# Performance work log

Measured on AMD Instinct MI355X. Metric: run time of the kernel, lower is better.

Reference implementation:

```python
import jax, jax.numpy as jnp
import numpy as np

K = 2          # kernel_size
STRIDE = 1
C_IN = 2       # n_channels (hardcoded in module)
NQ = K * K     # 4 qubits
PI = np.pi


def _apply_1q(state, gate, wire):
    # state: [N, 16] complex64; gate: [N,2,2] (batched) or [2,2] (shared)
    N = state.shape[0]
    s = state.reshape((N,) + (2,) * NQ)
    s = jnp.moveaxis(s, 1 + wire, NQ)          # wire axis -> last
    s = s.reshape(N, -1, 2)
    if gate.ndim == 3:
        s = jnp.einsum('nab,nkb->nka', gate, s)
    else:
        s = jnp.einsum('ab,nkb->nka', gate, s)
    s = s.reshape((N,) + (2,) * NQ)
    s = jnp.moveaxis(s, NQ, 1 + wire)
    return s.reshape(N, -1)


def _apply_cnot(state, ctrl, tgt):
    N = state.shape[0]
    s = state.reshape((N,) + (2,) * NQ)
    s = jnp.moveaxis(s, (1 + ctrl, 1 + tgt), (NQ - 1, NQ))
    shp = s.shape
    s = s.reshape(N, -1, 2, 2)                 # [..., ctrl, tgt]
    s = jnp.concatenate([s[:, :, :1, :], s[:, :, 1:, ::-1]], axis=2)
    s = s.reshape(shp)
    s = jnp.moveaxis(s, (NQ - 1, NQ), (1 + ctrl, 1 + tgt))
    return s.reshape(N, -1)


def _rx(theta):
    # theta: [N] or scalar -> [N,2,2] or [2,2] complex
    c = jnp.cos(theta / 2).astype(jnp.complex64)
    s = (-1j) * jnp.sin(theta / 2).astype(jnp.complex64)
    return jnp.stack([jnp.stack([c, s], -1), jnp.stack([s, c], -1)], -2)


def _ry(theta):
    c = jnp.cos(theta / 2)
    s = jnp.sin(theta / 2)
    return jnp.stack([jnp.stack([c, -s], -1), jnp.stack([s, c], -1)], -2).astype(jnp.complex64)


def _circuit(angles, weights):
    # angles: [N, 8]; weights: [L, 4]. Returns expval(PauliZ) per wire: [N, 4].
    N = angles.shape[0]
    state = jnp.zeros((N, 2 ** NQ), jnp.complex64).at[:, 0].set(1.0)
    for i in range(NQ):
        state = _apply_1q(state, _rx(angles[:, 2 * i]), i)
        state = _apply_1q(state, _ry(angles[:, 2 * i + 1]), i)
    # BasicEntanglerLayers: per layer RX(w[l,i]) on wire i, then CNOT ring
    for l in range(weights.shape[0]):
        for i in range(NQ):
            state = _apply_1q(state, _rx(weights[l, i]), i)
        for i in range(NQ):
            state = _apply_cnot(state, i, (i + 1) % NQ)
    p = state.real ** 2 + state.imag ** 2
    p = p.reshape((N,) + (2,) * NQ)
    ez = [jnp.sum(jnp.take(p, 0, axis=1 + w) - jnp.take(p, 1, axis=1 + w),
                  axis=tuple(range(1, NQ))) for w in range(NQ)]
    return jnp.stack(ez, -1)


def _forward(x, weights):
    B, C, H, W = x.shape
    nh = (H - K) // STRIDE + 1
    nw = (W - K) // STRIDE + 1
    # unfold: [B, C, nh, nw, K*K] with patch-element order (kh, kw)
    subs = [x[:, :, kh:kh + (nh - 1) * STRIDE + 1:STRIDE,
                    kw:kw + (nw - 1) * STRIDE + 1:STRIDE]
            for kh in range(K) for kw in range(K)]
    patches = jnp.stack(subs, axis=-1)                      # [B,C,nh,nw,KK]
    patches = patches.transpose(0, 2, 3, 4, 1)              # [B,nh,nw,KK,C]
    patches = patches.reshape(B, nh * nw, K * K * C)
    # per-sample min-max normalize to [0, pi]
    flat = patches.reshape(B, -1)
    pmin = flat.min(axis=1)[:, None, None]
    pmax = flat.max(axis=1)[:, None, None]
    angles = (patches - pmin) / (pmax - pmin + 1e-8) * PI
    angles = angles.reshape(B * nh * nw, K * K * C)
    out = _circuit(angles, weights)                         # [B*nh*nw, 4]
    return out.reshape(B, nh, nw, NQ).transpose(0, 3, 1, 2)


def setup_inputs() -> dict:
    key = jax.random.key(0)
    k1, k2 = jax.random.split(key)
    x = jax.random.normal(k1, (8, C_IN, 224, 224), dtype=jnp.float32)
    weights = jax.random.uniform(k2, (1, NQ), dtype=jnp.float32) * (2 * PI)
    return {"x": x, "weights": weights}


def reference(x, weights):
    return _forward(x, weights)
```

## Files before the change

### kernel.cpp

```cpp
#include <hip/hip_runtime.h>
#include <math.h>

#define BATCH 8
#define CIN   2
#define H     224
#define W     224
#define NH    223
#define NW    223
#define PIXB  (H * W)
#define NPB   (CIN * H * W)
#define PER_B (NH * NW)
#define NBPB  ((PER_B + 255) / 256)
#define BPB   32
#define PI_F  3.14159265358979323846f

__global__ __launch_bounds__(256) void minmax_kernel(
        const float* __restrict__ x, float* __restrict__ ws) {
    int b  = blockIdx.x / BPB;
    int cb = blockIdx.x % BPB;
    const float4* xb = (const float4*)(x + (size_t)b * NPB);
    const int n4  = NPB / 4;
    const int per = n4 / BPB;
    float lmin =  INFINITY, lmax = -INFINITY;
    for (int idx = cb * per + threadIdx.x; idx < (cb + 1) * per; idx += 256) {
        float4 v = xb[idx];
        lmin = fminf(lmin, fminf(fminf(v.x, v.y), fminf(v.z, v.w)));
        lmax = fmaxf(lmax, fmaxf(fmaxf(v.x, v.y), fmaxf(v.z, v.w)));
    }
    #pragma unroll
    for (int off = 32; off > 0; off >>= 1) {
        lmin = fminf(lmin, __shfl_down(lmin, off, 64));
        lmax = fmaxf(lmax, __shfl_down(lmax, off, 64));
    }
    __shared__ float smin[4], smax[4];
    int wid = threadIdx.x >> 6;
    if ((threadIdx.x & 63) == 0) { smin[wid] = lmin; smax[wid] = lmax; }
    __syncthreads();
    if (threadIdx.x == 0) {
        #pragma unroll
        for (int i = 1; i < 4; ++i) {
            lmin = fminf(lmin, smin[i]);
            lmax = fmaxf(lmax, smax[i]);
        }
        ws[b * BPB + cb]               = lmin;
        ws[256 + b * BPB + cb]         = lmax;
    }
}

__global__ __launch_bounds__(256) void quanv_kernel(
        const float* __restrict__ x, const float* __restrict__ wts,
        const float* __restrict__ ws, float* __restrict__ out) {
    int b = blockIdx.y;
    __shared__ float sred[2];
    if (threadIdx.x < 32) {
        float mn = ws[b * BPB + threadIdx.x];
        float mx = ws[256 + b * BPB + threadIdx.x];
        #pragma unroll
        for (int off = 16; off > 0; off >>= 1) {
            mn = fminf(mn, __shfl_xor(mn, off, 32));
            mx = fmaxf(mx, __shfl_xor(mx, off, 32));
        }
        if (threadIdx.x == 0) { sred[0] = mn; sred[1] = mx; }
    }
    __syncthreads();
    float gmin  = sred[0];
    float scale = PI_F / (sred[1] - gmin + 1e-8f);

    int r = blockIdx.x * 256 + threadIdx.x;
    if (r >= PER_B) return;
    int i = r / NW;
    int j = r - i * NW;

    const float* c0 = x + (size_t)b * NPB + (size_t)i * W + j;
    const float* c1 = c0 + PIXB;

    float z[4];
    #pragma unroll
    for (int q = 0; q < 4; ++q) {
        int kh = q >> 1, kw = q & 1;
        float pa = c0[kh * W + kw];
        float pb = c1[kh * W + kw];
        float a  = (pa - gmin) * scale;
        float bb = (pb - gmin) * scale;
        float sa, ca;
        __sincosf(a, &sa, &ca);
        float cb = __cosf(bb);
        float sw, cw;
        __sincosf(wts[q], &sw, &cw);
        z[q] = ca * cb * cw - sa * sw;
    }

    size_t base = (size_t)b * 4 * PER_B + r;
    float z01 = z[0] * z[1];
    out[base]             = z[1] * z[2] * z[3];
    out[base + PER_B]     = z01;
    out[base + 2 * PER_B] = z01 * z[2];
    out[base + 3 * PER_B] = z01 * z[2] * z[3];
}

extern "C" void kernel_launch(void* const* d_in, const int* in_sizes, int n_in,
                              void* d_out, int out_size, void* d_ws, size_t ws_size,
                              hipStream_t stream) {
    const float* x   = (const float*)d_in[0];
    const float* wts = (const float*)d_in[1];
    float* out = (float*)d_out;
    float* ws  = (float*)d_ws;

    minmax_kernel<<<BATCH * BPB, 256, 0, stream>>>(x, ws);
    quanv_kernel<<<dim3(NBPB, BATCH), 256, 0, stream>>>(x, wts, ws, out);
}
```

Measured before the change: 61.21 us.

## Fuse min-max reduction and quanv into one cooperative kernel with 4-wide pixel tiles

Replaces the two-kernel launch (min-max reduction, then quanv) with a single cooperative kernel that reduces, calls grid.sync, then computes the circuit output. Each thread now handles four adjacent output pixels, loading float4 rows and reusing trig values of shared patch columns, so redundant loads and sincos calls go away. Weight trig is precomputed once into the workspace. The cooperative launch needs all 392 blocks to be co-resident, and the grid barrier adds synchronisation cost.

```diff
diff --git a/kernel.cpp b/kernel.cpp
--- a/kernel.cpp
+++ b/kernel.cpp
@@ -1,5 +1,8 @@
 #include <hip/hip_runtime.h>
+#include <hip/hip_cooperative_groups.h>
 #include <math.h>
+
+namespace cg = cooperative_groups;
 
 #define BATCH 8
 #define CIN   2
@@ -10,92 +13,130 @@
 #define PIXB  (H * W)
 #define NPB   (CIN * H * W)
 #define PER_B (NH * NW)
-#define NBPB  ((PER_B + 255) / 256)
-#define BPB   32
+#define BPB2  49
+#define NBLK  (BATCH * BPB2)
+#define GPR   56
+#define SLOTS (NH * GPR)
 #define PI_F  3.14159265358979323846f
 
-__global__ __launch_bounds__(256) void minmax_kernel(
-        const float* __restrict__ x, float* __restrict__ ws) {
-    int b  = blockIdx.x / BPB;
-    int cb = blockIdx.x % BPB;
-    const float4* xb = (const float4*)(x + (size_t)b * NPB);
-    const int n4  = NPB / 4;
-    const int per = n4 / BPB;
-    float lmin =  INFINITY, lmax = -INFINITY;
-    for (int idx = cb * per + threadIdx.x; idx < (cb + 1) * per; idx += 256) {
-        float4 v = xb[idx];
-        lmin = fminf(lmin, fminf(fminf(v.x, v.y), fminf(v.z, v.w)));
-        lmax = fmaxf(lmax, fmaxf(fmaxf(v.x, v.y), fmaxf(v.z, v.w)));
+
+__global__ __launch_bounds__(256) void fused_quanv(
+        const float* __restrict__ x, const float* __restrict__ wts,
+        float* __restrict__ ws, float* __restrict__ out) {
+    cg::grid_group grid = cg::this_grid();
+    const int b  = blockIdx.x / BPB2;
+    const int cb = blockIdx.x - b * BPB2;
+
+    {
+        const float4* xb = (const float4*)(x + (size_t)b * NPB);
+        const int base = cb * 512 + threadIdx.x;
+        float4 v0 = xb[base];
+        float4 v1 = xb[base + 256];
+        float lmin = fminf(fminf(fminf(v0.x, v0.y), fminf(v0.z, v0.w)),
+                           fminf(fminf(v1.x, v1.y), fminf(v1.z, v1.w)));
+        float lmax = fmaxf(fmaxf(fmaxf(v0.x, v0.y), fmaxf(v0.z, v0.w)),
+                           fmaxf(fmaxf(v1.x, v1.y), fmaxf(v1.z, v1.w)));
+        #pragma unroll
+        for (int off = 32; off > 0; off >>= 1) {
+            lmin = fminf(lmin, __shfl_down(lmin, off, 64));
+            lmax = fmaxf(lmax, __shfl_down(lmax, off, 64));
+        }
+        __shared__ float smin[4], smax[4];
+        int wid = threadIdx.x >> 6;
+        if ((threadIdx.x & 63) == 0) { smin[wid] = lmin; smax[wid] = lmax; }
+        __syncthreads();
+        if (threadIdx.x == 0) {
+            #pragma unroll
+            for (int i = 1; i < 4; ++i) {
+                lmin = fminf(lmin, smin[i]);
+                lmax = fmaxf(lmax, smax[i]);
+            }
+            ws[blockIdx.x]       = lmin;
+            ws[512 + blockIdx.x] = lmax;
+        }
+        if (blockIdx.x == 0 && threadIdx.x < 4) {
+            float sw, cw;
+            __sincosf(wts[threadIdx.x], &sw, &cw);
+            ws[1024 + threadIdx.x] = cw;
+            ws[1028 + threadIdx.x] = sw;
+        }
     }
-    #pragma unroll
-    for (int off = 32; off > 0; off >>= 1) {
-        lmin = fminf(lmin, __shfl_down(lmin, off, 64));
-        lmax = fmaxf(lmax, __shfl_down(lmax, off, 64));
-    }
-    __shared__ float smin[4], smax[4];
-    int wid = threadIdx.x >> 6;
-    if ((threadIdx.x & 63) == 0) { smin[wid] = lmin; smax[wid] = lmax; }
-    __syncthreads();
-    if (threadIdx.x == 0) {
+
+    grid.sync();
+
+    __shared__ float sred[2];
+    if (threadIdx.x < 64) {
+        float mn = INFINITY, mx = -INFINITY;
+        if (threadIdx.x < BPB2) {
+            mn = ws[b * BPB2 + threadIdx.x];
+            mx = ws[512 + b * BPB2 + threadIdx.x];
+        }
         #pragma unroll
-        for (int i = 1; i < 4; ++i) {
-            lmin = fminf(lmin, smin[i]);
-            lmax = fmaxf(lmax, smax[i]);
-        }
-        ws[b * BPB + cb]               = lmin;
-        ws[256 + b * BPB + cb]         = lmax;
-    }
-}
-
-__global__ __launch_bounds__(256) void quanv_kernel(
-        const float* __restrict__ x, const float* __restrict__ wts,
-        const float* __restrict__ ws, float* __restrict__ out) {
-    int b = blockIdx.y;
-    __shared__ float sred[2];
-    if (threadIdx.x < 32) {
-        float mn = ws[b * BPB + threadIdx.x];
-        float mx = ws[256 + b * BPB + threadIdx.x];
-        #pragma unroll
-        for (int off = 16; off > 0; off >>= 1) {
-            mn = fminf(mn, __shfl_xor(mn, off, 32));
-            mx = fmaxf(mx, __shfl_xor(mx, off, 32));
+        for (int off = 32; off > 0; off >>= 1) {
+            mn = fminf(mn, __shfl_xor(mn, off, 64));
+            mx = fmaxf(mx, __shfl_xor(mx, off, 64));
         }
         if (threadIdx.x == 0) { sred[0] = mn; sred[1] = mx; }
     }
     __syncthreads();
-    float gmin  = sred[0];
-    float scale = PI_F / (sred[1] - gmin + 1e-8f);
+    const float gmin  = sred[0];
+    const float scale = PI_F / (sred[1] - gmin + 1e-8f);
 
-    int r = blockIdx.x * 256 + threadIdx.x;
-    if (r >= PER_B) return;
-    int i = r / NW;
-    int j = r - i * NW;
+    const float cw0 = ws[1024], cw1 = ws[1025], cw2 = ws[1026], cw3 = ws[1027];
+    const float sw0 = ws[1028], sw1 = ws[1029], sw2 = ws[1030], sw3 = ws[1031];
 
-    const float* c0 = x + (size_t)b * NPB + (size_t)i * W + j;
-    const float* c1 = c0 + PIXB;
+    const int g = cb * 256 + threadIdx.x;
+    if (g >= SLOTS) return;
+    const int i  = g / GPR;
+    const int jg = g - i * GPR;
+    const int j  = jg * 4;
+    const bool full = (j + 3 < NW);
 
-    float z[4];
-    #pragma unroll
-    for (int q = 0; q < 4; ++q) {
-        int kh = q >> 1, kw = q & 1;
-        float pa = c0[kh * W + kw];
-        float pb = c1[kh * W + kw];
-        float a  = (pa - gmin) * scale;
-        float bb = (pb - gmin) * scale;
-        float sa, ca;
-        __sincosf(a, &sa, &ca);
-        float cb = __cosf(bb);
-        float sw, cw;
-        __sincosf(wts[q], &sw, &cw);
-        z[q] = ca * cb * cw - sa * sw;
+    const float* r0 = x + (size_t)b * NPB + (size_t)i * W + j;
+    float4 p00 = *(const float4*)(r0);
+    float4 p01 = *(const float4*)(r0 + PIXB);
+    float4 p10 = *(const float4*)(r0 + W);
+    float4 p11 = *(const float4*)(r0 + W + PIXB);
+
+    float pcc[2][5], psa[2][5];
+    #define TRIG(pa, pb, PC, PS) do {                         \
+        float _a  = ((pa) - gmin) * scale;                    \
+        float _bb = ((pb) - gmin) * scale;                    \
+        float _s, _c; __sincosf(_a, &_s, &_c);                \
+        (PC) = _c * __cosf(_bb); (PS) = _s; } while (0)
+
+    TRIG(p00.x, p01.x, pcc[0][0], psa[0][0]);
+    TRIG(p00.y, p01.y, pcc[0][1], psa[0][1]);
+    TRIG(p00.z, p01.z, pcc[0][2], psa[0][2]);
+    TRIG(p00.w, p01.w, pcc[0][3], psa[0][3]);
+    TRIG(p10.x, p11.x, pcc[1][0], psa[1][0]);
+    TRIG(p10.y, p11.y, pcc[1][1], psa[1][1]);
+    TRIG(p10.z, p11.z, pcc[1][2], psa[1][2]);
+    TRIG(p10.w, p11.w, pcc[1][3], psa[1][3]);
+    if (full) {
+        float e0 = r0[4], e1 = (r0 + PIXB)[4];
+        float e2 = (r0 + W)[4], e3 = (r0 + W + PIXB)[4];
+        TRIG(e0, e1, pcc[0][4], psa[0][4]);
+        TRIG(e2, e3, pcc[1][4], psa[1][4]);
+    } else {
+        pcc[0][4] = psa[0][4] = pcc[1][4] = psa[1][4] = 0.0f;
     }
 
-    size_t base = (size_t)b * 4 * PER_B + r;
-    float z01 = z[0] * z[1];
-    out[base]             = z[1] * z[2] * z[3];
-    out[base + PER_B]     = z01;
-    out[base + 2 * PER_B] = z01 * z[2];
-    out[base + 3 * PER_B] = z01 * z[2] * z[3];
+    const int np = full ? 4 : 3;
+    const size_t obase = ((size_t)(b * 4) * NH + i) * NW + j;
+    #pragma unroll
+    for (int dj = 0; dj < 4; ++dj) {
+        if (dj >= np) break;
+        float z0 = pcc[0][dj]     * cw0 - psa[0][dj]     * sw0;
+        float z1 = pcc[0][dj + 1] * cw1 - psa[0][dj + 1] * sw1;
+        float z2 = pcc[1][dj]     * cw2 - psa[1][dj]     * sw2;
+        float z3 = pcc[1][dj + 1] * cw3 - psa[1][dj + 1] * sw3;
+        float z01 = z0 * z1;
+        out[obase + dj]             = z1 * z2 * z3;
+        out[obase + dj + PER_B]     = z01;
+        out[obase + dj + 2 * PER_B] = z01 * z2;
+        out[obase + dj + 3 * PER_B] = z01 * z2 * z3;
+    }
 }
 
 extern "C" void kernel_launch(void* const* d_in, const int* in_sizes, int n_in,
@@ -106,6 +147,7 @@
     float* out = (float*)d_out;
     float* ws  = (float*)d_ws;
 
-    minmax_kernel<<<BATCH * BPB, 256, 0, stream>>>(x, ws);
-    quanv_kernel<<<dim3(NBPB, BATCH), 256, 0, stream>>>(x, wts, ws, out);
+    void* args[] = { (void*)&x, (void*)&wts, (void*)&ws, (void*)&out };
+    hipLaunchCooperativeKernel((void*)fused_quanv, dim3(NBLK), dim3(256),
+                               args, 0, stream);
 }
```

Result: slower. 103.5 us (+69.0%).
